# Optimization experiments

Measured on AMD Instinct MI355X. Metric: run time of the kernel, lower is better.

The kernel has to match this reference:

```python
import jax, jax.numpy as jnp
import numpy as np

T = 32768       # sequence length
IN = 1024       # input_dim
HID = 512       # hidden_dim
OUT = 128       # output_dim
N_SUB = 4       # fixed RK4 substeps per odeint interval


def _uniform(key, shape, fan_in):
    s = 1.0 / np.sqrt(fan_in)
    return jax.random.uniform(key, shape, jnp.float32, -s, s)


def setup_inputs() -> dict:
    key = jax.random.key(0)
    ks = jax.random.split(key, 9)
    return {
        "t": jnp.arange(T, dtype=jnp.float32),
        "x": jax.random.normal(ks[0], (T, IN), jnp.float32),
        "W_in": _uniform(ks[1], (HID, IN), IN),
        "b_in": _uniform(ks[2], (HID,), IN),
        "W_h": _uniform(ks[3], (HID, HID), HID),
        "b_h": _uniform(ks[4], (HID,), HID),
        "W_ode": _uniform(ks[5], (HID, HID), HID),
        "b_ode": _uniform(ks[6], (HID,), HID),
        "W_dec": _uniform(ks[7], (OUT, HID), HID),
        "b_dec": _uniform(ks[8], (OUT,), HID),
    }


def reference(t, x, W_in, b_in, W_h, b_h, W_ode, b_ode, W_dec, b_dec):
    t = t.reshape(-1).astype(jnp.float32)

    def f(h):  # ODE_Func: tanh(Linear(h)); time-independent vector field
        return jnp.tanh(W_ode @ h + b_ode)

    def rk4_interval(h, dt_total):
        dt = dt_total / N_SUB
        def body(i, h):
            k1 = f(h)
            k2 = f(h + 0.5 * dt * k1)
            k3 = f(h + 0.5 * dt * k2)
            k4 = f(h + dt * k3)
            return h + (dt / 6.0) * (k1 + 2.0 * k2 + 2.0 * k3 + k4)
        return jax.lax.fori_loop(0, N_SUB, body, h)

    # i == 0: h_i = 0, so h = tanh(W_in x_0 + b_in + W_h @ 0 + b_h)
    h0 = jnp.tanh(W_in @ x[0] + b_in + b_h)

    def step(h, inp):
        x_i, dt = inp
        h_i = rk4_interval(h, dt)           # odeint(ode_func, h, [t_{i-1}, t_i])[1]
        h_new = jnp.tanh(W_in @ x_i + b_in + W_h @ h_i + b_h)
        return h_new, None

    dts = jnp.diff(t)                        # (T-1,)
    h, _ = jax.lax.scan(step, h0, (x[1:], dts))
    return W_dec @ h + b_dec                 # (OUT,)
```

## Files before the change

### kernel.cpp

```cpp
#include <hip/hip_runtime.h>
#include <stdint.h>

typedef _Float16 f16;
typedef f16 f16x2 __attribute__((ext_vector_type(2)));

#define T_LEN 32768
#define HID   512
#define IN_D  1024
#define OUT_D 128
#define NT    512
#define NBLK  4
#define RPB   128
#define SLICE_DW 32768

__device__ __forceinline__ float dot2f(uint32_t w, uint32_t v, float acc) {
    return __builtin_amdgcn_fdot2(__builtin_bit_cast(f16x2, w),
                                  __builtin_bit_cast(f16x2, v), acc, false);
}
__device__ __forceinline__ float fast_tanh(float z) {
    float e = __expf(2.f * z);
    return 1.f - 2.f * __builtin_amdgcn_rcpf(e + 1.f);
}

__global__ __launch_bounds__(NT) void k_prep(const float* __restrict__ W_ode,
                                             const float* __restrict__ W_h,
                                             uint32_t* __restrict__ ode_prep,
                                             uint32_t* __restrict__ wh_prep) {
    const int bid = blockIdx.x;
    const int c = bid & 3;
    const float* W = (bid >> 2) ? W_h : W_ode;
    uint4* dst = (uint4*)(((bid >> 2) ? wh_prep : ode_prep) + (size_t)c * SLICE_DW);
    const int t = threadIdx.x, rg = t >> 3, kg = t & 7;
    for (int j = 0; j < 16; ++j) {
        const int rl = j & 1, c8 = j >> 1;
        const int row = c * RPB + 2 * rg + rl;
        uint32_t cc[4];
#pragma unroll
        for (int mm = 0; mm < 4; ++mm) {
            const int k0 = kg * 64 + c8 * 8 + mm * 2;
            f16x2 pk;
            pk[0] = (f16)W[row * HID + k0];
            pk[1] = (f16)W[row * HID + k0 + 1];
            cc[mm] = __builtin_bit_cast(uint32_t, pk);
        }
        dst[j * NT + t] = uint4{cc[0], cc[1], cc[2], cc[3]};
    }
}

__global__ __launch_bounds__(512) void k_pre(const float* __restrict__ x,
                                             const float* __restrict__ W_in,
                                             const float* __restrict__ b_in,
                                             const float* __restrict__ b_h,
                                             float* __restrict__ pre32,
                                             uint16_t* __restrict__ pre16,
                                             int preF32) {
    __shared__ float xs[64][34];
    __shared__ float wsh[256][34];
    const int t  = threadIdx.x;
    const int i0 = (blockIdx.x >> 1) * 64;
    const int j0 = (blockIdx.x & 1) * 256;
    const int ti = t >> 5, tj = t & 31;

    float acc[4][8];
#pragma unroll
    for (int a = 0; a < 4; ++a)
#pragma unroll
        for (int b = 0; b < 8; ++b) acc[a][b] = 0.f;

    for (int kb = 0; kb < 32; ++kb) {
        __syncthreads();
        {
            int r = t >> 3, cc = (t & 7) * 4;
            float4 v = *(const float4*)&x[(size_t)(i0 + r) * IN_D + kb * 32 + cc];
            xs[r][cc] = v.x; xs[r][cc + 1] = v.y; xs[r][cc + 2] = v.z; xs[r][cc + 3] = v.w;
        }
        {
            int jr = t >> 1, c0 = (t & 1) * 16;
#pragma unroll
            for (int qd = 0; qd < 4; ++qd) {
                float4 v = *(const float4*)&W_in[(size_t)(j0 + jr) * IN_D + kb * 32 + c0 + qd * 4];
                wsh[jr][c0 + qd * 4]     = v.x; wsh[jr][c0 + qd * 4 + 1] = v.y;
                wsh[jr][c0 + qd * 4 + 2] = v.z; wsh[jr][c0 + qd * 4 + 3] = v.w;
            }
        }
        __syncthreads();
#pragma unroll 4
        for (int k = 0; k < 32; ++k) {
            float xv[4], wv[8];
#pragma unroll
            for (int ii = 0; ii < 4; ++ii) xv[ii] = xs[ti * 4 + ii][k];
#pragma unroll
            for (int jj = 0; jj < 8; ++jj) wv[jj] = wsh[tj + 32 * jj][k];
#pragma unroll
            for (int ii = 0; ii < 4; ++ii)
#pragma unroll
                for (int jj = 0; jj < 8; ++jj)
                    acc[ii][jj] = fmaf(xv[ii], wv[jj], acc[ii][jj]);
        }
    }
#pragma unroll
    for (int ii = 0; ii < 4; ++ii)
#pragma unroll
        for (int jj = 0; jj < 8; ++jj) {
            int ig = i0 + ti * 4 + ii, jg = j0 + tj + 32 * jj;
            float r = acc[ii][jj] + b_in[jg] + b_h[jg];
            if (preF32) pre32[(size_t)ig * HID + jg] = r;
            else        pre16[(size_t)ig * HID + jg] = __builtin_bit_cast(uint16_t, (f16)r);
        }
}

__global__ __launch_bounds__(NT) void k_scan(
    const uint32_t* __restrict__ ode_prep, const uint32_t* __restrict__ wh_prep,
    const float* __restrict__ pre32, const uint16_t* __restrict__ pre16, int preF32,
    const float* __restrict__ tarr, const float* __restrict__ b_ode,
    const float* __restrict__ W_dec, const float* __restrict__ b_dec,
    uint32_t* vx,
    float* __restrict__ out)
{
    __shared__ uint4 whlds[16 * NT];
    __shared__ __align__(16) uint16_t vbuf[2][576];

    const int c    = blockIdx.x;
    const int t    = threadIdx.x;
    const int rg   = t >> 3, kg = t & 7;
    const int lane = t & 63;
    const int wv   = t >> 6;
    const int rloc = 2 * rg + (kg & 1);
    const int row_glob = c * RPB + rloc;
    const uint4* o4 = (const uint4*)(ode_prep + (size_t)c * SLICE_DW);
    const uint4* h4 = (const uint4*)(wh_prep  + (size_t)c * SLICE_DW);

    uint32_t wreg[64];
#pragma unroll
    for (int j = 0; j < 16; ++j) {
        uint4 w = o4[j * NT + t];
        wreg[4 * j] = w.x; wreg[4 * j + 1] = w.y;
        wreg[4 * j + 2] = w.z; wreg[4 * j + 3] = w.w;
    }
#pragma unroll
    for (int j = 0; j < 16; ++j)
        whlds[j * NT + t] = h4[j * NT + t];

    const float bo = b_ode[row_glob];

    int cur = 1;
    uint32_t m = 0;

    auto reduceZ = [&](float a0, float a1) -> float {
        float mine = (kg & 1) ? a1 : a0;
        float oth  = (kg & 1) ? a0 : a1;
        float b = mine + __shfl_xor(oth, 1);
        b += __shfl_xor(b, 2);
        b += __shfl_xor(b, 4);
        return b;
    };

    auto mv_ode = [&]() -> float {
        float a0 = 0.f, a1 = 0.f;
        const char* vb = (const char*)&vbuf[cur][0] + kg * 144;
#pragma unroll
        for (int c8 = 0; c8 < 8; ++c8) {
            const uint4 vv = *(const uint4*)(vb + c8 * 16);
            const int j0 = (c8 * 2) * 4, j1 = (c8 * 2 + 1) * 4;
            a0 = dot2f(wreg[j0],     vv.x, a0);
            a0 = dot2f(wreg[j0 + 1], vv.y, a0);
            a0 = dot2f(wreg[j0 + 2], vv.z, a0);
            a0 = dot2f(wreg[j0 + 3], vv.w, a0);
            a1 = dot2f(wreg[j1],     vv.x, a1);
            a1 = dot2f(wreg[j1 + 1], vv.y, a1);
            a1 = dot2f(wreg[j1 + 2], vv.z, a1);
            a1 = dot2f(wreg[j1 + 3], vv.w, a1);
        }
        return reduceZ(a0, a1);
    };

    auto mv_wh = [&]() -> float {
        float a0 = 0.f, a1 = 0.f;
        const char* vb = (const char*)&vbuf[cur][0] + kg * 144;
#pragma unroll
        for (int c8 = 0; c8 < 8; ++c8) {
            const uint4 vv = *(const uint4*)(vb + c8 * 16);
            const uint4 w0 = whlds[(c8 * 2) * NT + t];
            const uint4 w1 = whlds[(c8 * 2 + 1) * NT + t];
            a0 = dot2f(w0.x, vv.x, a0); a0 = dot2f(w0.y, vv.y, a0);
            a0 = dot2f(w0.z, vv.z, a0); a0 = dot2f(w0.w, vv.w, a0);
            a1 = dot2f(w1.x, vv.x, a1); a1 = dot2f(w1.y, vv.y, a1);
            a1 = dot2f(w1.z, vv.z, a1); a1 = dot2f(w1.w, vv.w, a1);
        }
        return reduceZ(a0, a1);
    };

    auto pushx = [&](float n) {
        ++m;
        const uint32_t mt = m & 0xffffu;
        const int nxt = cur ^ 1;
        uint32_t* slot = vx + (m & 1) * 512;
        const uint16_t nb = __builtin_bit_cast(uint16_t, (f16)n);
        if (kg < 2) {
            vbuf[nxt][(row_glob >> 6) * 72 + (row_glob & 63)] = nb;
            __hip_atomic_store(&slot[c * RPB + rloc], (mt << 16) | (uint32_t)nb,
                               __ATOMIC_RELAXED, __HIP_MEMORY_SCOPE_AGENT);
        }
        if (wv >= 1 && wv <= 3) {
            const int fb = (c + wv) & 3;
            uint32_t* p0 = &slot[fb * RPB + lane];
            uint32_t d0, d1;
            for (;;) {
                d0 = __hip_atomic_load(p0,      __ATOMIC_RELAXED, __HIP_MEMORY_SCOPE_AGENT);
                d1 = __hip_atomic_load(p0 + 64, __ATOMIC_RELAXED, __HIP_MEMORY_SCOPE_AGENT);
                if (__all((d0 >> 16) == mt && (d1 >> 16) == mt)) break;
            }
            vbuf[nxt][(2 * fb) * 72 + lane]     = (uint16_t)d0;
            vbuf[nxt][(2 * fb + 1) * 72 + lane] = (uint16_t)d1;
        }
        __syncthreads();
        cur = nxt;
    };

    float h;
    {
        float p0 = preF32 ? pre32[row_glob] : (float)__builtin_bit_cast(f16, pre16[row_glob]);
        h = fast_tanh(p0);
    }
    pushx(h);
    float tprev = tarr[0];

#pragma unroll 1
    for (int i = 1; i < T_LEN; ++i) {
        float tc  = tarr[i];
        float dtt = tc - tprev; tprev = tc;
        float dt  = 0.25f * dtt;
        float hdt = 0.5f * dt;
        float sixth = dt * (1.f / 6.f);
        float pv = preF32 ? pre32[(size_t)i * HID + row_glob]
                          : (float)__builtin_bit_cast(f16, pre16[(size_t)i * HID + row_glob]);
#pragma unroll 1
        for (int sub = 0; sub < 4; ++sub) {
            float ks = 0.f;
#pragma unroll 1
            for (int s = 0; s < 4; ++s) {
                float z = mv_ode();
                float k = fast_tanh(z + bo);
                float wk = (s == 1 || s == 2) ? 2.f : 1.f;
                ks = fmaf(wk, k, ks);
                float n;
                if (s == 3) { h = fmaf(sixth, ks, h); n = h; }
                else        { float a = (s == 2) ? dt : hdt; n = fmaf(a, k, h); }
                pushx(n);
            }
        }
        float zh = mv_wh();
        h = fast_tanh(pv + zh);
        pushx(h);
    }

    if (c == 0 && t < OUT_D) {
        float a = b_dec[t];
#pragma unroll 4
        for (int k = 0; k < HID; ++k) {
            uint16_t hb = vbuf[cur][(k >> 6) * 72 + (k & 63)];
            a = fmaf(W_dec[t * HID + k], (float)__builtin_bit_cast(f16, hb), a);
        }
        out[t] = a;
    }
}

extern "C" void kernel_launch(void* const* d_in, const int* in_sizes, int n_in,
                              void* d_out, int out_size, void* d_ws, size_t ws_size,
                              hipStream_t stream) {
    const float* tarr  = (const float*)d_in[0];
    const float* x     = (const float*)d_in[1];
    const float* W_in  = (const float*)d_in[2];
    const float* b_in  = (const float*)d_in[3];
    const float* W_h   = (const float*)d_in[4];
    const float* b_h   = (const float*)d_in[5];
    const float* W_ode = (const float*)d_in[6];
    const float* b_ode = (const float*)d_in[7];
    const float* W_dec = (const float*)d_in[8];
    const float* b_dec = (const float*)d_in[9];
    float* out = (float*)d_out;

    uint8_t*  ws       = (uint8_t*)d_ws;
    uint32_t* ode_prep = (uint32_t*)(ws);
    uint32_t* wh_prep  = (uint32_t*)(ws + (512u << 10));
    uint32_t* vx       = (uint32_t*)(ws + (1u << 20));
    void*     pre      = (void*)(ws + (1u << 20) + 65536);

    size_t need32 = (1u << 20) + 65536 + (size_t)T_LEN * HID * 4 + 4096;
    int preF32 = (ws_size >= need32) ? 1 : 0;

    hipMemsetAsync(vx, 0, 4096, stream);
    hipLaunchKernelGGL(k_prep, dim3(8), dim3(NT), 0, stream, W_ode, W_h, ode_prep, wh_prep);
    hipLaunchKernelGGL(k_pre,  dim3(1024), dim3(512), 0, stream, x, W_in, b_in, b_h,
                       (float*)pre, (uint16_t*)pre, preF32);
    hipLaunchKernelGGL(k_scan, dim3(NBLK), dim3(NT), 0, stream, ode_prep, wh_prep,
                       (const float*)pre, (const uint16_t*)pre, preF32,
                       tarr, b_ode, W_dec, b_dec, vx, out);
}
```

Measured before the change: 594.5 ms.

## Co-locate scan blocks on one XCC and poll peers with L2-scope loads

The scan kernel now launches 25 blocks and keeps only every eighth one as a worker. The intent is that round-robin dispatch places all four workers on the same XCC. Each worker records its XCC id and checks whether all four match; if so, it polls peer hidden-state slots with sc0 global loads that are coherent at the shared L2, instead of agent-scope atomics that go further out. Polling is also split across six wavefronts, each waiting on one 64-entry half, and there is a fallback after many failed tries. This is meant to cut the latency of the per-step cross-block exchange, but it depends on how the hardware dispatches blocks and on inline asm coherence behaviour.

```diff
diff --git a/kernel.cpp b/kernel.cpp
--- a/kernel.cpp
+++ b/kernel.cpp
@@ -9,7 +9,7 @@
 #define IN_D  1024
 #define OUT_D 128
 #define NT    512
-#define NBLK  4
+#define NWORK 4
 #define RPB   128
 #define SLICE_DW 32768
 
@@ -20,6 +20,13 @@
 __device__ __forceinline__ float fast_tanh(float z) {
     float e = __expf(2.f * z);
     return 1.f - 2.f * __builtin_amdgcn_rcpf(e + 1.f);
+}
+__device__ __forceinline__ uint32_t ld_sc0(const uint32_t* p) {
+    uint32_t d;
+    asm volatile("global_load_dword %0, %1, off sc0\n\t"
+                 "s_waitcnt vmcnt(0)"
+                 : "=&v"(d) : "v"((uint64_t)p) : "memory");
+    return d;
 }
 
 __global__ __launch_bounds__(NT) void k_prep(const float* __restrict__ W_ode,
@@ -117,10 +124,14 @@
     uint32_t* vx,
     float* __restrict__ out)
 {
+    const int bid = blockIdx.x;
+    if (bid & 7) return;
+    const int c = bid >> 3;
+
     __shared__ uint4 whlds[16 * NT];
     __shared__ __align__(16) uint16_t vbuf[2][576];
-
-    const int c    = blockIdx.x;
+    __shared__ int s_fast;
+
     const int t    = threadIdx.x;
     const int rg   = t >> 3, kg = t & 7;
     const int lane = t & 63;
@@ -130,6 +141,25 @@
     const uint4* o4 = (const uint4*)(ode_prep + (size_t)c * SLICE_DW);
     const uint4* h4 = (const uint4*)(wh_prep  + (size_t)c * SLICE_DW);
 
+    if (t == 0) {
+        int xcc;
+        asm volatile("s_getreg_b32 %0, hwreg(HW_REG_XCC_ID)" : "=s"(xcc));
+        __hip_atomic_store(&vx[1024 + c], 0x100u | (uint32_t)(xcc & 0xff),
+                           __ATOMIC_RELAXED, __HIP_MEMORY_SCOPE_AGENT);
+        uint32_t e[4];
+        for (;;) {
+            bool ok = true;
+#pragma unroll
+            for (int b = 0; b < 4; ++b) {
+                e[b] = __hip_atomic_load(&vx[1024 + b], __ATOMIC_RELAXED,
+                                         __HIP_MEMORY_SCOPE_AGENT);
+                ok = ok && ((e[b] & 0x100u) != 0);
+            }
+            if (ok) break;
+        }
+        s_fast = (e[0] == e[1] && e[1] == e[2] && e[2] == e[3]) ? 1 : 0;
+    }
+
     uint32_t wreg[64];
 #pragma unroll
     for (int j = 0; j < 16; ++j) {
@@ -142,6 +172,8 @@
         whlds[j * NT + t] = h4[j * NT + t];
 
     const float bo = b_ode[row_glob];
+    __syncthreads();
+    int fastp = s_fast;
 
     int cur = 1;
     uint32_t m = 0;
@@ -201,17 +233,21 @@
             __hip_atomic_store(&slot[c * RPB + rloc], (mt << 16) | (uint32_t)nb,
                                __ATOMIC_RELAXED, __HIP_MEMORY_SCOPE_AGENT);
         }
-        if (wv >= 1 && wv <= 3) {
-            const int fb = (c + wv) & 3;
-            uint32_t* p0 = &slot[fb * RPB + lane];
-            uint32_t d0, d1;
+        if (wv >= 1 && wv <= 6) {
+            const int task = wv - 1;
+            const int fb   = (c + 1 + (task >> 1)) & 3;
+            const int half = task & 1;
+            const uint32_t* p0 = &slot[fb * RPB + half * 64 + lane];
+            uint32_t d0;
+            int tries = 0;
             for (;;) {
-                d0 = __hip_atomic_load(p0,      __ATOMIC_RELAXED, __HIP_MEMORY_SCOPE_AGENT);
-                d1 = __hip_atomic_load(p0 + 64, __ATOMIC_RELAXED, __HIP_MEMORY_SCOPE_AGENT);
-                if (__all((d0 >> 16) == mt && (d1 >> 16) == mt)) break;
+                d0 = fastp ? ld_sc0(p0)
+                           : __hip_atomic_load(p0, __ATOMIC_RELAXED,
+                                               __HIP_MEMORY_SCOPE_AGENT);
+                if (__all((d0 >> 16) == mt)) break;
+                if (fastp && ++tries > 2048) fastp = 0;
             }
-            vbuf[nxt][(2 * fb) * 72 + lane]     = (uint16_t)d0;
-            vbuf[nxt][(2 * fb + 1) * 72 + lane] = (uint16_t)d1;
+            vbuf[nxt][(2 * fb + half) * 72 + lane] = (uint16_t)d0;
         }
         __syncthreads();
         cur = nxt;
@@ -289,11 +325,11 @@
     size_t need32 = (1u << 20) + 65536 + (size_t)T_LEN * HID * 4 + 4096;
     int preF32 = (ws_size >= need32) ? 1 : 0;
 
-    hipMemsetAsync(vx, 0, 4096, stream);
+    hipMemsetAsync(vx, 0, 8192, stream);
     hipLaunchKernelGGL(k_prep, dim3(8), dim3(NT), 0, stream, W_ode, W_h, ode_prep, wh_prep);
     hipLaunchKernelGGL(k_pre,  dim3(1024), dim3(512), 0, stream, x, W_in, b_in, b_h,
                        (float*)pre, (uint16_t*)pre, preF32);
-    hipLaunchKernelGGL(k_scan, dim3(NBLK), dim3(NT), 0, stream, ode_prep, wh_prep,
+    hipLaunchKernelGGL(k_scan, dim3(25), dim3(NT), 0, stream, ode_prep, wh_prep,
                        (const float*)pre, (const uint16_t*)pre, preF32,
                        tarr, b_ode, W_dec, b_dec, vx, out);
 }
```

Result: faster. 541.1 ms (-9.0%).
